# Performance work log

Hardware: AMD Instinct MI355X
Metric: run time of the kernel (lower is better)

## Reference

```python
import jax, jax.numpy as jnp
import numpy as np

N = 50000
E = 800000
IN_DIM = 512
H1 = IN_DIM // 2   # 256
H2 = IN_DIM // 4   # 128
D = 8
NP_CAYLEY = D * (D - 1) // 2  # 28


def setup_inputs() -> dict:
    key = jax.random.key(0)
    ks = jax.random.split(key, 10)
    x = jax.random.normal(ks[0], (N, IN_DIM), dtype=jnp.float32)
    edge_index = jax.random.randint(ks[1], (2, E), 0, N, dtype=jnp.int64)
    s1 = 1.0 / np.sqrt(IN_DIM)
    s2 = 1.0 / np.sqrt(H1)
    s3 = 1.0 / np.sqrt(H2)
    W1l = jax.random.uniform(ks[2], (H1, IN_DIM), jnp.float32, -s1, s1)
    b1 = jax.random.uniform(ks[3], (H1,), jnp.float32, -s1, s1)
    W1r = jax.random.uniform(ks[4], (H1, IN_DIM), jnp.float32, -s1, s1)
    W2l = jax.random.uniform(ks[5], (H2, H1), jnp.float32, -s2, s2)
    b2 = jax.random.uniform(ks[6], (H2,), jnp.float32, -s2, s2)
    W2r = jax.random.uniform(ks[7], (H2, H1), jnp.float32, -s2, s2)
    Wp = jax.random.uniform(ks[8], (NP_CAYLEY, H2), jnp.float32, -s3, s3)
    bp = jax.random.uniform(ks[9], (NP_CAYLEY,), jnp.float32, -s3, s3)
    return {"x": x, "edge_index": edge_index,
            "W1l": W1l, "b1": b1, "W1r": W1r,
            "W2l": W2l, "b2": b2, "W2r": W2r,
            "Wp": Wp, "bp": bp}


def _sage_conv(x, src, dst, Wl, bl, Wr):
    # PyG SAGEConv (mean aggr): out = lin_l(mean_{j in N(i)} x_j) + lin_r(x_i)
    msg_sum = jax.ops.segment_sum(x[src], dst, num_segments=N)  # [N, F]
    deg = jax.ops.segment_sum(jnp.ones((src.shape[0],), x.dtype), dst,
                              num_segments=N)
    mean = msg_sum / jnp.maximum(deg, 1.0)[:, None]
    return mean @ Wl.T + bl + x @ Wr.T


def _cayley(params):
    # params: [N, d(d-1)/2] -> skew A, then O = (I - A)^{-1} (I + A)
    iu, ju = jnp.triu_indices(D, k=1)  # row-major i<j matches torch loop order
    n = params.shape[0]
    A = jnp.zeros((n, D, D), params.dtype)
    A = A.at[:, iu, ju].set(params)
    A = A.at[:, ju, iu].set(-params)
    I = jnp.eye(D, dtype=params.dtype)
    return jnp.linalg.solve(I[None] - A, I[None] + A)


def reference(x, edge_index, W1l, b1, W1r, W2l, b2, W2r, Wp, bp):
    src, dst = edge_index[0], edge_index[1]
    h = jax.nn.relu(_sage_conv(x, src, dst, W1l, b1, W1r))
    h = jax.nn.relu(_sage_conv(h, src, dst, W2l, b2, W2r))
    params = h @ Wp.T + bp  # [N, 28]
    return _cayley(params)  # [N, 8, 8]
```

## Files before the change

### kernel.cpp

```cpp
#include <hip/hip_runtime.h>
#include <hip/hip_bf16.h>


#define WS_ALIGN(x) (((x) + 255) & ~size_t(255))

typedef __attribute__((ext_vector_type(8))) short short8;
typedef __attribute__((ext_vector_type(4))) float floatx4;

static __device__ __forceinline__ ushort f2b(float f) {
    unsigned u = __builtin_bit_cast(unsigned, f);
    u = (u + 0x7fffu + ((u >> 16) & 1u)) >> 16;
    return (ushort)u;
}
static __device__ __forceinline__ float b2f(ushort h) {
    unsigned u = ((unsigned)h) << 16;
    return __builtin_bit_cast(float, u);
}


__global__ void hist_kernel(const int* __restrict__ dst, int* __restrict__ deg, int E) {
    int e = blockIdx.x * blockDim.x + threadIdx.x;
    if (e < E) atomicAdd(&deg[dst[e]], 1);
}

__global__ __launch_bounds__(256)
void scan_phase1(const int* __restrict__ deg, int* __restrict__ bsum, int n) {
    __shared__ int red[256];
    const int t = threadIdx.x;
    const int i = blockIdx.x * 1024 + t * 4;
    int s = 0;
    if (i + 4 <= n) {
        int4 v = *reinterpret_cast<const int4*>(&deg[i]);
        s = v.x + v.y + v.z + v.w;
    } else {
        for (int k = i; k < n; ++k) s += deg[k];
    }
    red[t] = s;
    __syncthreads();
#pragma unroll
    for (int off = 128; off > 0; off >>= 1) {
        if (t < off) red[t] += red[t + off];
        __syncthreads();
    }
    if (t == 0) bsum[blockIdx.x] = red[0];
}

__global__ __launch_bounds__(256)
void scan_phase2(int* __restrict__ bsum, int* __restrict__ rowptr, int nb, int n) {
    __shared__ int sh[256];
    const int t = threadIdx.x;
    int orig = (t < nb) ? bsum[t] : 0;
    sh[t] = orig;
    __syncthreads();
#pragma unroll
    for (int off = 1; off < 256; off <<= 1) {
        int v = (t >= off) ? sh[t - off] : 0;
        __syncthreads();
        sh[t] += v;
        __syncthreads();
    }
    if (t < nb) bsum[t] = sh[t] - orig;
    if (t == 255) rowptr[n] = sh[255];
}

__global__ __launch_bounds__(256)
void scan_phase3(const int* __restrict__ deg, const int* __restrict__ bsum,
                 int* __restrict__ rowptr, int n) {
    __shared__ int red[256];
    const int t = threadIdx.x;
    const int i = blockIdx.x * 1024 + t * 4;
    int v0 = 0, v1 = 0, v2 = 0, v3 = 0;
    if (i + 4 <= n) {
        int4 v = *reinterpret_cast<const int4*>(&deg[i]);
        v0 = v.x; v1 = v.y; v2 = v.z; v3 = v.w;
    } else {
        if (i     < n) v0 = deg[i];
        if (i + 1 < n) v1 = deg[i + 1];
        if (i + 2 < n) v2 = deg[i + 2];
        if (i + 3 < n) v3 = deg[i + 3];
    }
    int s = v0 + v1 + v2 + v3;
    red[t] = s;
    __syncthreads();
#pragma unroll
    for (int off = 1; off < 256; off <<= 1) {
        int u = (t >= off) ? red[t - off] : 0;
        __syncthreads();
        red[t] += u;
        __syncthreads();
    }
    int pre = bsum[blockIdx.x] + red[t] - s;
    if (i + 4 <= n) {
        int4 o;
        o.x = pre; o.y = pre + v0; o.z = pre + v0 + v1; o.w = pre + v0 + v1 + v2;
        *reinterpret_cast<int4*>(&rowptr[i]) = o;
    } else {
        if (i     < n) rowptr[i]     = pre;
        if (i + 1 < n) rowptr[i + 1] = pre + v0;
        if (i + 2 < n) rowptr[i + 2] = pre + v0 + v1;
        if (i + 3 < n) rowptr[i + 3] = pre + v0 + v1 + v2;
    }
}

__global__ void scatter_kernel(const int* __restrict__ src, const int* __restrict__ dst,
                               const int* __restrict__ rowptr, int* __restrict__ cursor,
                               int* __restrict__ adj, int E) {
    int e = blockIdx.x * blockDim.x + threadIdx.x;
    if (e < E) {
        int d = dst[e];
        int p = atomicAdd(&cursor[d], 1);
        adj[rowptr[d] + p] = src[e];
    }
}


__global__ void cast_kernel(const float* __restrict__ src, ushort* __restrict__ dst, int n8) {
    for (int i = blockIdx.x * blockDim.x + threadIdx.x; i < n8; i += gridDim.x * blockDim.x) {
        const float4* s4 = reinterpret_cast<const float4*>(src + (size_t)i * 8);
        float4 v0 = s4[0], v1 = s4[1];
        short8 o;
        o[0] = (short)f2b(v0.x); o[1] = (short)f2b(v0.y);
        o[2] = (short)f2b(v0.z); o[3] = (short)f2b(v0.w);
        o[4] = (short)f2b(v1.x); o[5] = (short)f2b(v1.y);
        o[6] = (short)f2b(v1.z); o[7] = (short)f2b(v1.w);
        *reinterpret_cast<short8*>(dst + (size_t)i * 8) = o;
    }
}

__global__ void build_wcat(const float* __restrict__ W1l, const float* __restrict__ W1r,
                           const float* __restrict__ W2l, const float* __restrict__ W2r,
                           ushort* __restrict__ Wc1, ushort* __restrict__ Wc2) {
    int idx = blockIdx.x * blockDim.x + threadIdx.x;
    const int n1 = (512 * 512) / 8;
    const int n2 = (256 * 256) / 8;
    const float* src;
    ushort* dst;
    if (idx < n1) {
        int e = idx * 8;
        int row = e >> 9, col = e & 511;
        src = (row < 256) ? &W1l[row * 512 + col] : &W1r[(row - 256) * 512 + col];
        dst = &Wc1[e];
    } else if (idx < n1 + n2) {
        int e = (idx - n1) * 8;
        int row = e >> 8, col = e & 255;
        src = (row < 128) ? &W2l[row * 256 + col] : &W2r[(row - 128) * 256 + col];
        dst = &Wc2[e];
    } else {
        return;
    }
    const float4* s4 = reinterpret_cast<const float4*>(src);
    float4 v0 = s4[0], v1 = s4[1];
    short8 o;
    o[0] = (short)f2b(v0.x); o[1] = (short)f2b(v0.y);
    o[2] = (short)f2b(v0.z); o[3] = (short)f2b(v0.w);
    o[4] = (short)f2b(v1.x); o[5] = (short)f2b(v1.y);
    o[6] = (short)f2b(v1.z); o[7] = (short)f2b(v1.w);
    *reinterpret_cast<short8*>(dst) = o;
}


__global__ __launch_bounds__(256)
void gemm_bf16(const ushort* __restrict__ A, const ushort* __restrict__ B,
               ushort* __restrict__ C, int M, int K, int Ncols) {
    __shared__ ushort As[128 * 64];
    __shared__ ushort Bs[128 * 64];
    const int tid  = threadIdx.x;
    const int wave = tid >> 6;
    const int lane = tid & 63;
    const int row0 = blockIdx.y * 128;
    const int col0 = blockIdx.x * 128;
    const int wm = (wave & 1) * 64;
    const int wn = (wave >> 1) * 64;

    floatx4 acc[4][4];
#pragma unroll
    for (int i = 0; i < 4; ++i)
#pragma unroll
        for (int j = 0; j < 4; ++j)
            acc[i][j] = (floatx4){0.f, 0.f, 0.f, 0.f};

    const int rsub = lane >> 3;
    const int ksw  = ((lane & 7) * 16) ^ (rsub << 4);

    for (int k0 = 0; k0 < K; k0 += 64) {
#pragma unroll
        for (int i = 0; i < 4; ++i) {
            int chunk = wave * 4 + i;
            int r = chunk * 8 + rsub;
            int grow = row0 + r;
            if (grow >= M) grow = M - 1;
            const char* src = (const char*)(A + (size_t)grow * K + k0) + ksw;
            __builtin_amdgcn_global_load_lds(
                (const __attribute__((address_space(1))) unsigned int*)src,
                (__attribute__((address_space(3))) unsigned int*)(&As[chunk * 512]),
                16, 0, 0);
        }
#pragma unroll
        for (int i = 0; i < 4; ++i) {
            int chunk = wave * 4 + i;
            int r = chunk * 8 + rsub;
            int gcol = col0 + r;
            const char* src = (const char*)(B + (size_t)gcol * K + k0) + ksw;
            __builtin_amdgcn_global_load_lds(
                (const __attribute__((address_space(1))) unsigned int*)src,
                (__attribute__((address_space(3))) unsigned int*)(&Bs[chunk * 512]),
                16, 0, 0);
        }
        __syncthreads();

#pragma unroll
        for (int kk = 0; kk < 2; ++kk) {
            short8 af[4], bf[4];
            const int kb = (kk * 64 + ((lane >> 4) << 4)) ^ ((lane & 7) << 4);
#pragma unroll
            for (int im = 0; im < 4; ++im) {
                int r = wm + im * 16 + (lane & 15);
                af[im] = *reinterpret_cast<const short8*>((const char*)As + r * 128 + kb);
            }
#pragma unroll
            for (int in = 0; in < 4; ++in) {
                int r = wn + in * 16 + (lane & 15);
                bf[in] = *reinterpret_cast<const short8*>((const char*)Bs + r * 128 + kb);
            }
#pragma unroll
            for (int im = 0; im < 4; ++im)
#pragma unroll
                for (int in = 0; in < 4; ++in)
                    acc[im][in] = __builtin_amdgcn_mfma_f32_16x16x32_bf16(
                        af[im], bf[in], acc[im][in], 0, 0, 0);
        }
        __syncthreads();
    }

#pragma unroll
    for (int im = 0; im < 4; ++im) {
#pragma unroll
        for (int reg = 0; reg < 4; ++reg) {
            int r = row0 + wm + im * 16 + ((lane >> 4) << 2) + reg;
            if (r < M) {
                size_t base = (size_t)r * Ncols + col0 + wn + (lane & 15);
#pragma unroll
                for (int in = 0; in < 4; ++in)
                    C[base + in * 16] = f2b(acc[im][in][reg]);
            }
        }
    }
}


template <int LPN>
__global__ __launch_bounds__(256)
void aggregate_bf16(const ushort* __restrict__ Y, const float* __restrict__ bias,
                    const int* __restrict__ rowptr, const int* __restrict__ adj,
                    ushort* __restrict__ H, int n) {
    constexpr int F = LPN * 4;
    const int grp = threadIdx.x / LPN;
    const int sub = threadIdx.x % LPN;
    const int node = blockIdx.x * (256 / LPN) + grp;
    if (node >= n) return;
    const int c = sub * 4;
    const int start = rowptr[node], end = rowptr[node + 1];
    const int twoF = 2 * F;

    float a0 = 0.f, a1 = 0.f, a2 = 0.f, a3 = 0.f;
    int e = start;
    for (; e + 4 <= end; e += 4) {
        int s0 = adj[e + 0], s1 = adj[e + 1], s2 = adj[e + 2], s3 = adj[e + 3];
        ushort4 r0 = *reinterpret_cast<const ushort4*>(&Y[(size_t)s0 * twoF + c]);
        ushort4 r1 = *reinterpret_cast<const ushort4*>(&Y[(size_t)s1 * twoF + c]);
        ushort4 r2 = *reinterpret_cast<const ushort4*>(&Y[(size_t)s2 * twoF + c]);
        ushort4 r3 = *reinterpret_cast<const ushort4*>(&Y[(size_t)s3 * twoF + c]);
        a0 += (b2f(r0.x) + b2f(r1.x)) + (b2f(r2.x) + b2f(r3.x));
        a1 += (b2f(r0.y) + b2f(r1.y)) + (b2f(r2.y) + b2f(r3.y));
        a2 += (b2f(r0.z) + b2f(r1.z)) + (b2f(r2.z) + b2f(r3.z));
        a3 += (b2f(r0.w) + b2f(r1.w)) + (b2f(r2.w) + b2f(r3.w));
    }
    for (; e < end; ++e) {
        int s = adj[e];
        ushort4 r = *reinterpret_cast<const ushort4*>(&Y[(size_t)s * twoF + c]);
        a0 += b2f(r.x); a1 += b2f(r.y); a2 += b2f(r.z); a3 += b2f(r.w);
    }

    const int d = end - start;
    const float inv = 1.0f / (float)(d > 0 ? d : 1);
    ushort4 sv = *reinterpret_cast<const ushort4*>(&Y[(size_t)node * twoF + F + c]);
    float4 bv = *reinterpret_cast<const float4*>(&bias[c]);
    ushort4 o;
    o.x = f2b(fmaxf(a0 * inv + b2f(sv.x) + bv.x, 0.f));
    o.y = f2b(fmaxf(a1 * inv + b2f(sv.y) + bv.y, 0.f));
    o.z = f2b(fmaxf(a2 * inv + b2f(sv.z) + bv.z, 0.f));
    o.w = f2b(fmaxf(a3 * inv + b2f(sv.w) + bv.w, 0.f));
    *reinterpret_cast<ushort4*>(&H[(size_t)node * F + c]) = o;
}


__global__ __launch_bounds__(256)
void final_kernel(const ushort* __restrict__ H2, const float* __restrict__ Wp,
                  const float* __restrict__ bp, float* __restrict__ Out, int n) {
    __shared__ float WpS[28 * 128];
    __shared__ float bpS[28];
    for (int t = threadIdx.x; t < 28 * 128; t += 256) WpS[t] = Wp[t];
    if (threadIdx.x < 28) bpS[threadIdx.x] = bp[threadIdx.x];
    __syncthreads();

    int i = blockIdx.x * blockDim.x + threadIdx.x;
    if (i >= n) return;

    float p[28];
#pragma unroll
    for (int j = 0; j < 28; ++j) p[j] = bpS[j];
    const short8* hp = reinterpret_cast<const short8*>(&H2[(size_t)i * 128]);
#pragma unroll
    for (int q = 0; q < 16; ++q) {
        short8 hv = hp[q];
        float h[8];
#pragma unroll
        for (int t = 0; t < 8; ++t) h[t] = b2f((ushort)hv[t]);
#pragma unroll
        for (int j = 0; j < 28; ++j) {
            const float* w = &WpS[j * 128 + 8 * q];
            float s = 0.f;
#pragma unroll
            for (int t = 0; t < 8; ++t) s += h[t] * w[t];
            p[j] += s;
        }
    }

    float M_[8][8], B_[8][8];
#pragma unroll
    for (int r = 0; r < 8; ++r)
#pragma unroll
        for (int c = 0; c < 8; ++c) {
            M_[r][c] = (r == c) ? 1.f : 0.f;
            B_[r][c] = (r == c) ? 1.f : 0.f;
        }
    {
        int idx = 0;
#pragma unroll
        for (int r = 0; r < 8; ++r)
#pragma unroll
            for (int c = r + 1; c < 8; ++c) {
                float a = p[idx++];
                M_[r][c] -= a;  M_[c][r] += a;
                B_[r][c] += a;  B_[c][r] -= a;
            }
    }
#pragma unroll
    for (int col = 0; col < 8; ++col) {
        float inv = 1.0f / M_[col][col];
#pragma unroll
        for (int c = 0; c < 8; ++c) { M_[col][c] *= inv; B_[col][c] *= inv; }
#pragma unroll
        for (int r = 0; r < 8; ++r) {
            if (r == col) continue;
            float f = M_[r][col];
#pragma unroll
            for (int c = 0; c < 8; ++c) {
                M_[r][c] -= f * M_[col][c];
                B_[r][c] -= f * B_[col][c];
            }
        }
    }
    float* out = &Out[(size_t)i * 64];
#pragma unroll
    for (int r = 0; r < 8; ++r) {
        float4 o0 = make_float4(B_[r][0], B_[r][1], B_[r][2], B_[r][3]);
        float4 o1 = make_float4(B_[r][4], B_[r][5], B_[r][6], B_[r][7]);
        *reinterpret_cast<float4*>(&out[r * 8 + 0]) = o0;
        *reinterpret_cast<float4*>(&out[r * 8 + 4]) = o1;
    }
}


extern "C" void kernel_launch(void* const* d_in, const int* in_sizes, int n_in,
                              void* d_out, int out_size, void* d_ws, size_t ws_size,
                              hipStream_t stream) {
    const float* x   = (const float*)d_in[0];
    const int*   ei  = (const int*)d_in[1];
    const float* W1l = (const float*)d_in[2];
    const float* b1  = (const float*)d_in[3];
    const float* W1r = (const float*)d_in[4];
    const float* W2l = (const float*)d_in[5];
    const float* b2  = (const float*)d_in[6];
    const float* W2r = (const float*)d_in[7];
    const float* Wp  = (const float*)d_in[8];
    const float* bp  = (const float*)d_in[9];
    float* out = (float*)d_out;

    const int IN_DIM = 512;
    const int N = in_sizes[0] / IN_DIM;
    const int E = in_sizes[1] / 2;

    char* ws = (char*)d_ws;
    size_t off = 0;
    int* deg      = (int*)(ws + off); off = WS_ALIGN(off + (size_t)N * 4);
    int* rowptr   = (int*)(ws + off); off = WS_ALIGN(off + (size_t)(N + 1) * 4);
    int* cursor   = (int*)(ws + off); off = WS_ALIGN(off + (size_t)N * 4);
    int* bsum     = (int*)(ws + off); off = WS_ALIGN(off + (size_t)256 * 4);
    int* adj      = (int*)(ws + off); off = WS_ALIGN(off + (size_t)E * 4);
    ushort* xb    = (ushort*)(ws + off); off = WS_ALIGN(off + (size_t)N * 512 * 2);
    ushort* Y     = (ushort*)(ws + off); off = WS_ALIGN(off + (size_t)N * 512 * 2);
    ushort* h1    = (ushort*)(ws + off); off = WS_ALIGN(off + (size_t)N * 256 * 2);
    ushort* Wc1   = (ushort*)(ws + off); off = WS_ALIGN(off + (size_t)512 * 512 * 2);
    ushort* Wc2   = (ushort*)(ws + off); off = WS_ALIGN(off + (size_t)256 * 256 * 2);

    const int* src = ei;
    const int* dst = ei + E;

    hipMemsetAsync(deg, 0, (size_t)N * 4, stream);
    hipMemsetAsync(cursor, 0, (size_t)N * 4, stream);

    int eb = (E + 255) / 256;
    int nb = (N + 1023) / 1024;
    hist_kernel<<<eb, 256, 0, stream>>>(dst, deg, E);
    scan_phase1<<<nb, 256, 0, stream>>>(deg, bsum, N);
    scan_phase2<<<1, 256, 0, stream>>>(bsum, rowptr, nb, N);
    scan_phase3<<<nb, 256, 0, stream>>>(deg, bsum, rowptr, N);
    scatter_kernel<<<eb, 256, 0, stream>>>(src, dst, rowptr, cursor, adj, E);

    cast_kernel<<<1024, 256, 0, stream>>>(x, xb, N * 512 / 8);
    build_wcat<<<((512 * 512 + 256 * 256) / 8 + 255) / 256, 256, 0, stream>>>(
        W1l, W1r, W2l, W2r, Wc1, Wc2);

    int gm = (N + 127) / 128;

    gemm_bf16<<<dim3(4, gm), 256, 0, stream>>>(xb, Wc1, Y, N, 512, 512);
    aggregate_bf16<64><<<(N + 3) / 4, 256, 0, stream>>>(Y, b1, rowptr, adj, h1, N);

    ushort* zb = xb;
    gemm_bf16<<<dim3(2, gm), 256, 0, stream>>>(h1, Wc2, zb, N, 256, 256);
    ushort* h2 = Y;
    aggregate_bf16<32><<<(N + 7) / 8, 256, 0, stream>>>(zb, b2, rowptr, adj, h2, N);

    final_kernel<<<(N + 255) / 256, 256, 0, stream>>>(h2, Wp, bp, out, N);
}
```

Baseline: 324.9 us.

## Split GEMM output into separate left/right buffers and split final projection kernel

```diff
diff --git a/kernel.cpp b/kernel.cpp
--- a/kernel.cpp
+++ b/kernel.cpp
@@ -161,7 +161,8 @@
 
 __global__ __launch_bounds__(256)
 void gemm_bf16(const ushort* __restrict__ A, const ushort* __restrict__ B,
-               ushort* __restrict__ C, int M, int K, int Ncols) {
+               ushort* __restrict__ Cl, ushort* __restrict__ Cr,
+               int M, int K, int Ncols, int S) {
     __shared__ ushort As[128 * 64];
     __shared__ ushort Bs[128 * 64];
     const int tid  = threadIdx.x;
@@ -232,16 +233,18 @@
         __syncthreads();
     }
 
+    ushort* Cbase = (col0 < S) ? Cl : Cr;
+    const int cb = (col0 < S) ? col0 : col0 - S;
 #pragma unroll
     for (int im = 0; im < 4; ++im) {
 #pragma unroll
         for (int reg = 0; reg < 4; ++reg) {
             int r = row0 + wm + im * 16 + ((lane >> 4) << 2) + reg;
             if (r < M) {
-                size_t base = (size_t)r * Ncols + col0 + wn + (lane & 15);
+                size_t base = (size_t)r * S + cb + wn + (lane & 15);
 #pragma unroll
                 for (int in = 0; in < 4; ++in)
-                    C[base + in * 16] = f2b(acc[im][in][reg]);
+                    Cbase[base + in * 16] = f2b(acc[im][in][reg]);
             }
         }
     }
@@ -250,7 +253,8 @@
 
 template <int LPN>
 __global__ __launch_bounds__(256)
-void aggregate_bf16(const ushort* __restrict__ Y, const float* __restrict__ bias,
+void aggregate_bf16(const ushort* __restrict__ Yl, const ushort* __restrict__ Yr,
+                    const float* __restrict__ bias,
                     const int* __restrict__ rowptr, const int* __restrict__ adj,
                     ushort* __restrict__ H, int n) {
     constexpr int F = LPN * 4;
@@ -260,16 +264,15 @@
     if (node >= n) return;
     const int c = sub * 4;
     const int start = rowptr[node], end = rowptr[node + 1];
-    const int twoF = 2 * F;
 
     float a0 = 0.f, a1 = 0.f, a2 = 0.f, a3 = 0.f;
     int e = start;
     for (; e + 4 <= end; e += 4) {
         int s0 = adj[e + 0], s1 = adj[e + 1], s2 = adj[e + 2], s3 = adj[e + 3];
-        ushort4 r0 = *reinterpret_cast<const ushort4*>(&Y[(size_t)s0 * twoF + c]);
-        ushort4 r1 = *reinterpret_cast<const ushort4*>(&Y[(size_t)s1 * twoF + c]);
-        ushort4 r2 = *reinterpret_cast<const ushort4*>(&Y[(size_t)s2 * twoF + c]);
-        ushort4 r3 = *reinterpret_cast<const ushort4*>(&Y[(size_t)s3 * twoF + c]);
+        ushort4 r0 = *reinterpret_cast<const ushort4*>(&Yl[(size_t)s0 * F + c]);
+        ushort4 r1 = *reinterpret_cast<const ushort4*>(&Yl[(size_t)s1 * F + c]);
+        ushort4 r2 = *reinterpret_cast<const ushort4*>(&Yl[(size_t)s2 * F + c]);
+        ushort4 r3 = *reinterpret_cast<const ushort4*>(&Yl[(size_t)s3 * F + c]);
         a0 += (b2f(r0.x) + b2f(r1.x)) + (b2f(r2.x) + b2f(r3.x));
         a1 += (b2f(r0.y) + b2f(r1.y)) + (b2f(r2.y) + b2f(r3.y));
         a2 += (b2f(r0.z) + b2f(r1.z)) + (b2f(r2.z) + b2f(r3.z));
@@ -277,13 +280,13 @@
     }
     for (; e < end; ++e) {
         int s = adj[e];
-        ushort4 r = *reinterpret_cast<const ushort4*>(&Y[(size_t)s * twoF + c]);
+        ushort4 r = *reinterpret_cast<const ushort4*>(&Yl[(size_t)s * F + c]);
         a0 += b2f(r.x); a1 += b2f(r.y); a2 += b2f(r.z); a3 += b2f(r.w);
     }
 
     const int d = end - start;
     const float inv = 1.0f / (float)(d > 0 ? d : 1);
-    ushort4 sv = *reinterpret_cast<const ushort4*>(&Y[(size_t)node * twoF + F + c]);
+    ushort4 sv = *reinterpret_cast<const ushort4*>(&Yr[(size_t)node * F + c]);
     float4 bv = *reinterpret_cast<const float4*>(&bias[c]);
     ushort4 o;
     o.x = f2b(fmaxf(a0 * inv + b2f(sv.x) + bv.x, 0.f));
@@ -295,35 +298,63 @@
 
 
 __global__ __launch_bounds__(256)
-void final_kernel(const ushort* __restrict__ H2, const float* __restrict__ Wp,
-                  const float* __restrict__ bp, float* __restrict__ Out, int n) {
-    __shared__ float WpS[28 * 128];
-    __shared__ float bpS[28];
-    for (int t = threadIdx.x; t < 28 * 128; t += 256) WpS[t] = Wp[t];
-    if (threadIdx.x < 28) bpS[threadIdx.x] = bp[threadIdx.x];
+void params_kernel(const ushort* __restrict__ H2, const float* __restrict__ Wp,
+                   const float* __restrict__ bp, float* __restrict__ P, int n) {
+    __shared__ float WpS[32 * 132];
+    __shared__ float bpS[32];
+    for (int t = threadIdx.x; t < 32 * 132; t += 256) WpS[t] = 0.f;
+    if (threadIdx.x < 32) bpS[threadIdx.x] = (threadIdx.x < 28) ? bp[threadIdx.x] : 0.f;
     __syncthreads();
-
+    for (int t = threadIdx.x; t < 28 * 128; t += 256) {
+        int r = t >> 7, c = t & 127;
+        WpS[r * 132 + c] = Wp[t];
+    }
+    __syncthreads();
+
+    const int node = blockIdx.x * 32 + (threadIdx.x >> 3);
+    const int l = threadIdx.x & 7;
+    if (node >= n) return;
+
+    short8 h8[16];
+    const short8* hp = reinterpret_cast<const short8*>(&H2[(size_t)node * 128]);
+#pragma unroll
+    for (int q = 0; q < 16; ++q) h8[q] = hp[q];
+
+    float acc0 = bpS[l], acc1 = bpS[l + 8], acc2 = bpS[l + 16], acc3 = bpS[l + 24];
+#pragma unroll
+    for (int q = 0; q < 32; ++q) {
+        float h0 = b2f((ushort)h8[q >> 1][(q & 1) * 4 + 0]);
+        float h1 = b2f((ushort)h8[q >> 1][(q & 1) * 4 + 1]);
+        float h2 = b2f((ushort)h8[q >> 1][(q & 1) * 4 + 2]);
+        float h3 = b2f((ushort)h8[q >> 1][(q & 1) * 4 + 3]);
+        float4 w0 = *reinterpret_cast<const float4*>(&WpS[(l +  0) * 132 + 4 * q]);
+        float4 w1 = *reinterpret_cast<const float4*>(&WpS[(l +  8) * 132 + 4 * q]);
+        float4 w2 = *reinterpret_cast<const float4*>(&WpS[(l + 16) * 132 + 4 * q]);
+        float4 w3 = *reinterpret_cast<const float4*>(&WpS[(l + 24) * 132 + 4 * q]);
+        acc0 += h0 * w0.x + h1 * w0.y + h2 * w0.z + h3 * w0.w;
+        acc1 += h0 * w1.x + h1 * w1.y + h2 * w1.z + h3 * w1.w;
+        acc2 += h0 * w2.x + h1 * w2.y + h2 * w2.z + h3 * w2.w;
+        acc3 += h0 * w3.x + h1 * w3.y + h2 * w3.z + h3 * w3.w;
+    }
+    float* pout = &P[(size_t)node * 32];
+    pout[l]      = acc0;
+    pout[l + 8]  = acc1;
+    pout[l + 16] = acc2;
+    pout[l + 24] = acc3;
+}
+
+
+__global__ __launch_bounds__(256)
+void cayley_kernel(const float* __restrict__ P, float* __restrict__ Out, int n) {
     int i = blockIdx.x * blockDim.x + threadIdx.x;
     if (i >= n) return;
-
     float p[28];
-#pragma unroll
-    for (int j = 0; j < 28; ++j) p[j] = bpS[j];
-    const short8* hp = reinterpret_cast<const short8*>(&H2[(size_t)i * 128]);
-#pragma unroll
-    for (int q = 0; q < 16; ++q) {
-        short8 hv = hp[q];
-        float h[8];
-#pragma unroll
-        for (int t = 0; t < 8; ++t) h[t] = b2f((ushort)hv[t]);
-#pragma unroll
-        for (int j = 0; j < 28; ++j) {
-            const float* w = &WpS[j * 128 + 8 * q];
-            float s = 0.f;
-#pragma unroll
-            for (int t = 0; t < 8; ++t) s += h[t] * w[t];
-            p[j] += s;
-        }
+    const float4* pp = reinterpret_cast<const float4*>(&P[(size_t)i * 32]);
+#pragma unroll
+    for (int q = 0; q < 7; ++q) {
+        float4 v = pp[q];
+        p[4 * q + 0] = v.x; p[4 * q + 1] = v.y;
+        p[4 * q + 2] = v.z; p[4 * q + 3] = v.w;
     }
 
     float M_[8][8], B_[8][8];
@@ -399,10 +430,12 @@
     int* bsum     = (int*)(ws + off); off = WS_ALIGN(off + (size_t)256 * 4);
     int* adj      = (int*)(ws + off); off = WS_ALIGN(off + (size_t)E * 4);
     ushort* xb    = (ushort*)(ws + off); off = WS_ALIGN(off + (size_t)N * 512 * 2);
-    ushort* Y     = (ushort*)(ws + off); off = WS_ALIGN(off + (size_t)N * 512 * 2);
+    ushort* Yl    = (ushort*)(ws + off); off = WS_ALIGN(off + (size_t)N * 256 * 2);
+    ushort* Yr    = (ushort*)(ws + off); off = WS_ALIGN(off + (size_t)N * 256 * 2);
     ushort* h1    = (ushort*)(ws + off); off = WS_ALIGN(off + (size_t)N * 256 * 2);
     ushort* Wc1   = (ushort*)(ws + off); off = WS_ALIGN(off + (size_t)512 * 512 * 2);
     ushort* Wc2   = (ushort*)(ws + off); off = WS_ALIGN(off + (size_t)256 * 256 * 2);
+    float*  Pp    = (float*)(ws + off);  off = WS_ALIGN(off + (size_t)N * 32 * 4);
 
     const int* src = ei;
     const int* dst = ei + E;
@@ -424,13 +457,15 @@
 
     int gm = (N + 127) / 128;
 
-    gemm_bf16<<<dim3(4, gm), 256, 0, stream>>>(xb, Wc1, Y, N, 512, 512);
-    aggregate_bf16<64><<<(N + 3) / 4, 256, 0, stream>>>(Y, b1, rowptr, adj, h1, N);
-
-    ushort* zb = xb;
-    gemm_bf16<<<dim3(2, gm), 256, 0, stream>>>(h1, Wc2, zb, N, 256, 256);
-    ushort* h2 = Y;
-    aggregate_bf16<32><<<(N + 7) / 8, 256, 0, stream>>>(zb, b2, rowptr, adj, h2, N);
-
-    final_kernel<<<(N + 255) / 256, 256, 0, stream>>>(h2, Wp, bp, out, N);
-}
+    gemm_bf16<<<dim3(4, gm), 256, 0, stream>>>(xb, Wc1, Yl, Yr, N, 512, 512, 256);
+    aggregate_bf16<64><<<(N + 3) / 4, 256, 0, stream>>>(Yl, Yr, b1, rowptr, adj, h1, N);
+
+    ushort* zl = xb;
+    ushort* zr = xb + (size_t)N * 128;
+    gemm_bf16<<<dim3(2, gm), 256, 0, stream>>>(h1, Wc2, zl, zr, N, 256, 256, 128);
+    ushort* h2 = Yl;
+    aggregate_bf16<32><<<(N + 7) / 8, 256, 0, stream>>>(zl, zr, b2, rowptr, adj, h2, N);
+
+    params_kernel<<<(N + 31) / 32, 256, 0, stream>>>(h2, Wp, bp, Pp, N);
+    cayley_kernel<<<(N + 255) / 256, 256, 0, stream>>>(Pp, out, N);
+}
```

New measurement: 301.5 us. 7.2% less time.
